# Kernel tuning notes

Measured on AMD Instinct MI355X. Metric: run time of the kernel, lower is better.

Reference implementation:

```python
import jax, jax.numpy as jnp
import numpy as np

CONV_DIMS = (-3, -2)   # spatial dims (channel-last layout)
RADIUS = (3, 3)        # window = 1 + 2*r = 7 per dim -> 49 cells
STEP = (1, 1)


def _unfold(x, dim, window, step):
    """torch.Tensor.unfold: dim -> out_len, window appended as last axis."""
    dim = dim % x.ndim
    n = x.shape[dim]
    starts = jnp.arange((n - window) // step + 1) * step          # [L]
    idx = starts[:, None] + jnp.arange(window)[None, :]           # [L, w]
    y = jnp.take(x, idx, axis=dim)                                # dim -> [L, w]
    return jnp.moveaxis(y, dim + 1, -1)                           # window axis to last


def _local_attention(x):
    # Unfold each conv dim; move its window axis to the front (as in the torch code).
    for i, r, s in zip(CONV_DIMS, RADIUS, STEP):
        x = _unfold(x, i, 1 + 2 * r, s)
        x = jnp.moveaxis(x, -1, 0)
    n_win = len(CONV_DIMS)
    cells = int(np.prod(x.shape[:n_win]))
    x = x.reshape((cells,) + x.shape[n_win:])      # [cells, B, H', W', C]
    center = cells // 2                            # spatial center of the window
    q = jnp.moveaxis(x[center:center + 1], 0, -2)  # [B, H', W', 1, C]
    k = jnp.moveaxis(jnp.concatenate([x[:center], x[center + 1:]], axis=0), 0, -2)  # [B,H',W',cells-1,C]
    d = q.shape[-1]
    scores = jnp.einsum('...qc,...kc->...qk', q, k) / jnp.sqrt(jnp.asarray(d, q.dtype))
    w = jax.nn.softmax(scores, axis=-1)
    out = jnp.einsum('...qk,...kc->...qc', w, k)   # keys double as values
    return out.squeeze(-2)                          # [B, H', W', C]


def setup_inputs() -> dict:
    key = jax.random.key(0)
    X = jax.random.normal(key, (4, 64, 64, 256), dtype=jnp.float32)
    return {"X": X}


def reference(X):
    return _local_attention(X)
```

## Files before the change

### kernel.cpp

```cpp
#include <hip/hip_runtime.h>

#define B_   4
#define H_   64
#define W_   64
#define C_   256
#define HO_  58
#define WO_  58
#define TI_  29
#define TJ_  29
#define GRID (B_ * TI_ * TJ_)

template <int CTRL>
__device__ __forceinline__ float dpp_add(float p) {
    int t = __builtin_amdgcn_update_dpp(0, __builtin_bit_cast(int, p),
                                        CTRL, 0xF, 0xF, true);
    return p + __builtin_bit_cast(float, t);
}
__device__ __forceinline__ float reduce32_dpp(float p) {
    p = dpp_add<0x111>(p);
    p = dpp_add<0x112>(p);
    p = dpp_add<0x114>(p);
    p = dpp_add<0x118>(p);
    p = dpp_add<0x142>(p);
    return p;
}

__device__ __forceinline__ float dot8(const float4& k0, const float4& k1,
                                      const float4& q0, const float4& q1) {
    float s = k0.x * q0.x;
    s = fmaf(k0.y, q0.y, s); s = fmaf(k0.z, q0.z, s); s = fmaf(k0.w, q0.w, s);
    s = fmaf(k1.x, q1.x, s); s = fmaf(k1.y, q1.y, s); s = fmaf(k1.z, q1.z, s);
    s = fmaf(k1.w, q1.w, s);
    return s;
}

__global__ __launch_bounds__(256, 4) void convnd_attn_kernel(const float* __restrict__ X,
                                                             float* __restrict__ out) {
    __shared__ float sS[4][64];
    __shared__ float sW[4][64];
    __shared__ __align__(16) float pacc[4][8][C_];

    const int xcd = blockIdx.x & 7;
    const int bt  = blockIdx.x >> 3;
    const int sp  = (xcd < 4) ? (xcd * 421 + bt) : (4 * 421 + (xcd - 4) * 420 + bt);
    const int tj  = sp % TJ_;
    const int tmp = sp / TJ_;
    const int ti  = tmp % TI_;
    const int b   = tmp / TI_;
    const int i0  = 2 * ti;
    const int j0  = 2 * tj;

    const int tid  = threadIdx.x;
    const int wave = tid >> 6;
    const int lane = tid & 63;
    const int g    = lane >> 5;
    const int sub  = lane & 31;
    const int slot = wave * 2 + g;
    const int co   = 8 * sub;

    const float* base = X + (size_t)b * (H_ * W_ * C_);

    float4 kv[8][2];
    #pragma unroll
    for (int r = 0; r < 8; ++r) {
        const float* kp = base + ((i0 + r) * W_ + (j0 + slot)) * C_ + co;
        kv[r][0] = *(const float4*)(kp);
        kv[r][1] = *(const float4*)(kp + 4);
    }

    float4 q[4][2];
    #pragma unroll
    for (int p = 0; p < 4; ++p) {
        const int a = p >> 1, c = p & 1;
        const float* qp = base + ((i0 + a + 3) * W_ + (j0 + c + 3)) * C_ + co;
        float4 q0 = *(const float4*)(qp);
        float4 q1 = *(const float4*)(qp + 4);
        q0.x *= 0.0625f; q0.y *= 0.0625f; q0.z *= 0.0625f; q0.w *= 0.0625f;
        q1.x *= 0.0625f; q1.y *= 0.0625f; q1.z *= 0.0625f; q1.w *= 0.0625f;
        q[p][0] = q0; q[p][1] = q1;
    }

    #pragma unroll
    for (int r = 0; r < 8; ++r) {
        #pragma unroll
        for (int p = 0; p < 4; ++p) {
            float s = dot8(kv[r][0], kv[r][1], q[p][0], q[p][1]);
            s = reduce32_dpp(s);
            if (sub == 31) sS[p][r * 8 + slot] = s;
        }
    }
    __syncthreads();

    {
        const int p  = wave;
        const int a  = p >> 1, c = p & 1;
        const int di = lane >> 3, dj = lane & 7;
        const bool valid = (di >= a) & (di <= a + 6) & (dj >= c) & (dj <= c + 6)
                           & !((di == a + 3) & (dj == c + 3));
        const float e = valid ? __expf(sS[p][lane]) : 0.f;
        float ts = e;
        #pragma unroll
        for (int m = 32; m; m >>= 1) ts += __shfl_xor(ts, m, 64);
        sW[p][lane] = e / ts;
    }
    __syncthreads();

    float4 acc[4][2];
    #pragma unroll
    for (int p = 0; p < 4; ++p) {
        acc[p][0] = make_float4(0.f, 0.f, 0.f, 0.f);
        acc[p][1] = make_float4(0.f, 0.f, 0.f, 0.f);
    }
    #pragma unroll
    for (int r = 0; r < 8; ++r) {
        #pragma unroll
        for (int p = 0; p < 4; ++p) {
            const float w = sW[p][r * 8 + slot];
            acc[p][0].x = fmaf(w, kv[r][0].x, acc[p][0].x);
            acc[p][0].y = fmaf(w, kv[r][0].y, acc[p][0].y);
            acc[p][0].z = fmaf(w, kv[r][0].z, acc[p][0].z);
            acc[p][0].w = fmaf(w, kv[r][0].w, acc[p][0].w);
            acc[p][1].x = fmaf(w, kv[r][1].x, acc[p][1].x);
            acc[p][1].y = fmaf(w, kv[r][1].y, acc[p][1].y);
            acc[p][1].z = fmaf(w, kv[r][1].z, acc[p][1].z);
            acc[p][1].w = fmaf(w, kv[r][1].w, acc[p][1].w);
        }
    }
    #pragma unroll
    for (int p = 0; p < 4; ++p) {
        *(float4*)&pacc[p][slot][co]     = acc[p][0];
        *(float4*)&pacc[p][slot][co + 4] = acc[p][1];
    }
    __syncthreads();

    #pragma unroll
    for (int p = 0; p < 4; ++p) {
        float s = 0.f;
        #pragma unroll
        for (int sl = 0; sl < 8; ++sl) s += pacc[p][sl][tid];
        const int a = p >> 1, c = p & 1;
        out[(((size_t)b * HO_ + (i0 + a)) * WO_ + (j0 + c)) * C_ + tid] = s;
    }
}

extern "C" void kernel_launch(void* const* d_in, const int* in_sizes, int n_in,
                              void* d_out, int out_size, void* d_ws, size_t ws_size,
                              hipStream_t stream) {
    const float* X = (const float*)d_in[0];
    float* outp    = (float*)d_out;
    hipLaunchKernelGGL(convnd_attn_kernel,
                       dim3(GRID), dim3(256), 0, stream, X, outp);
}
```

Before: 88.70 us.

## Split key rows across two wave halves with 512-thread blocks

Doubles the block to 512 threads so each half of the waves handles four of the eight key rows. This halves the per-thread key registers and FMA work. Partial accumulators from the two halves are merged in shared memory, which adds a barrier and an LDS read-modify-write pass. The final reduction and store are spread over all 512 threads. The aim is more latency hiding and lower register pressure, at the cost of extra synchronization and some idle waves during the softmax step.

Result: no change. 89.66 us (+1.1%).

```diff
diff --git a/kernel.cpp b/kernel.cpp
--- a/kernel.cpp
+++ b/kernel.cpp
@@ -34,7 +34,7 @@
     return s;
 }
 
-__global__ __launch_bounds__(256, 4) void convnd_attn_kernel(const float* __restrict__ X,
+__global__ __launch_bounds__(512, 4) void convnd_attn_kernel(const float* __restrict__ X,
                                                              float* __restrict__ out) {
     __shared__ float sS[4][64];
     __shared__ float sW[4][64];
@@ -55,15 +55,17 @@
     const int lane = tid & 63;
     const int g    = lane >> 5;
     const int sub  = lane & 31;
-    const int slot = wave * 2 + g;
+    const int rh   = wave >> 2;
+    const int col  = 2 * (wave & 3) + g;
     const int co   = 8 * sub;
 
     const float* base = X + (size_t)b * (H_ * W_ * C_);
 
-    float4 kv[8][2];
+    float4 kv[4][2];
     #pragma unroll
-    for (int r = 0; r < 8; ++r) {
-        const float* kp = base + ((i0 + r) * W_ + (j0 + slot)) * C_ + co;
+    for (int r = 0; r < 4; ++r) {
+        const int row = rh * 4 + r;
+        const float* kp = base + ((i0 + row) * W_ + (j0 + col)) * C_ + co;
         kv[r][0] = *(const float4*)(kp);
         kv[r][1] = *(const float4*)(kp + 4);
     }
@@ -81,17 +83,17 @@
     }
 
     #pragma unroll
-    for (int r = 0; r < 8; ++r) {
+    for (int r = 0; r < 4; ++r) {
         #pragma unroll
         for (int p = 0; p < 4; ++p) {
             float s = dot8(kv[r][0], kv[r][1], q[p][0], q[p][1]);
             s = reduce32_dpp(s);
-            if (sub == 31) sS[p][r * 8 + slot] = s;
+            if (sub == 31) sS[p][(rh * 4 + r) * 8 + col] = s;
         }
     }
     __syncthreads();
 
-    {
+    if (wave < 4) {
         const int p  = wave;
         const int a  = p >> 1, c = p & 1;
         const int di = lane >> 3, dj = lane & 7;
@@ -112,10 +114,10 @@
         acc[p][1] = make_float4(0.f, 0.f, 0.f, 0.f);
     }
     #pragma unroll
-    for (int r = 0; r < 8; ++r) {
+    for (int r = 0; r < 4; ++r) {
         #pragma unroll
         for (int p = 0; p < 4; ++p) {
-            const float w = sW[p][r * 8 + slot];
+            const float w = sW[p][(rh * 4 + r) * 8 + col];
             acc[p][0].x = fmaf(w, kv[r][0].x, acc[p][0].x);
             acc[p][0].y = fmaf(w, kv[r][0].y, acc[p][0].y);
             acc[p][0].z = fmaf(w, kv[r][0].z, acc[p][0].z);
@@ -126,20 +128,38 @@
             acc[p][1].w = fmaf(w, kv[r][1].w, acc[p][1].w);
         }
     }
-    #pragma unroll
-    for (int p = 0; p < 4; ++p) {
-        *(float4*)&pacc[p][slot][co]     = acc[p][0];
-        *(float4*)&pacc[p][slot][co + 4] = acc[p][1];
+
+    if (rh == 1) {
+        #pragma unroll
+        for (int p = 0; p < 4; ++p) {
+            *(float4*)&pacc[p][col][co]     = acc[p][0];
+            *(float4*)&pacc[p][col][co + 4] = acc[p][1];
+        }
+    }
+    __syncthreads();
+    if (rh == 0) {
+        #pragma unroll
+        for (int p = 0; p < 4; ++p) {
+            float4 t0 = *(const float4*)&pacc[p][col][co];
+            float4 t1 = *(const float4*)&pacc[p][col][co + 4];
+            t0.x += acc[p][0].x; t0.y += acc[p][0].y; t0.z += acc[p][0].z; t0.w += acc[p][0].w;
+            t1.x += acc[p][1].x; t1.y += acc[p][1].y; t1.z += acc[p][1].z; t1.w += acc[p][1].w;
+            *(float4*)&pacc[p][col][co]     = t0;
+            *(float4*)&pacc[p][col][co + 4] = t1;
+        }
     }
     __syncthreads();
 
+    const int ch = tid & 255;
+    const int ph = tid >> 8;
     #pragma unroll
-    for (int p = 0; p < 4; ++p) {
+    for (int pp = 0; pp < 2; ++pp) {
+        const int p = pp * 2 + ph;
         float s = 0.f;
         #pragma unroll
-        for (int sl = 0; sl < 8; ++sl) s += pacc[p][sl][tid];
+        for (int sl = 0; sl < 8; ++sl) s += pacc[p][sl][ch];
         const int a = p >> 1, c = p & 1;
-        out[(((size_t)b * HO_ + (i0 + a)) * WO_ + (j0 + c)) * C_ + tid] = s;
+        out[(((size_t)b * HO_ + (i0 + a)) * WO_ + (j0 + c)) * C_ + ch] = s;
     }
 }
 
@@ -149,5 +169,5 @@
     const float* X = (const float*)d_in[0];
     float* outp    = (float*)d_out;
     hipLaunchKernelGGL(convnd_attn_kernel,
-                       dim3(GRID), dim3(256), 0, stream, X, outp);
+                       dim3(GRID), dim3(512), 0, stream, X, outp);
 }
```

## Compute local attention with split-bf16 MFMA over 2x8 output tiles

Applied to the files above, without the earlier changes.

Each block now handles a 2x8 tile of output pixels instead of 2x2. It loads the shared 8x16 key/value patch into LDS as hi/lo bf16 pairs and computes both the scores and the weighted sum with 16x16x32 bf16 MFMA, using three products per step to emulate fp32 precision. The larger tile reuses each loaded key row across more queries and moves the dot products onto matrix cores. In exchange it adds split and convert work, swizzled LDS traffic, more barriers and lower occupancy, and the dropped lo*lo term slightly reduces precision. The last column tile overlaps the previous one (j0=50) and recomputes a few pixels.

Result: slower. 102.5 us (+15.5%).

```diff
diff --git a/kernel.cpp b/kernel.cpp
--- a/kernel.cpp
+++ b/kernel.cpp
@@ -7,139 +7,233 @@
 #define HO_  58
 #define WO_  58
 #define TI_  29
-#define TJ_  29
+#define TJ_  8
 #define GRID (B_ * TI_ * TJ_)
 
-template <int CTRL>
-__device__ __forceinline__ float dpp_add(float p) {
-    int t = __builtin_amdgcn_update_dpp(0, __builtin_bit_cast(int, p),
-                                        CTRL, 0xF, 0xF, true);
-    return p + __builtin_bit_cast(float, t);
-}
-__device__ __forceinline__ float reduce32_dpp(float p) {
-    p = dpp_add<0x111>(p);
-    p = dpp_add<0x112>(p);
-    p = dpp_add<0x114>(p);
-    p = dpp_add<0x118>(p);
-    p = dpp_add<0x142>(p);
-    return p;
-}
-
-__device__ __forceinline__ float dot8(const float4& k0, const float4& k1,
-                                      const float4& q0, const float4& q1) {
-    float s = k0.x * q0.x;
-    s = fmaf(k0.y, q0.y, s); s = fmaf(k0.z, q0.z, s); s = fmaf(k0.w, q0.w, s);
-    s = fmaf(k1.x, q1.x, s); s = fmaf(k1.y, q1.y, s); s = fmaf(k1.z, q1.z, s);
-    s = fmaf(k1.w, q1.w, s);
-    return s;
-}
-
-__global__ __launch_bounds__(256, 4) void convnd_attn_kernel(const float* __restrict__ X,
+typedef __attribute__((ext_vector_type(8))) short bf16x8;
+typedef __attribute__((ext_vector_type(4))) float f32x4;
+
+__device__ __forceinline__ void split2(float a, float b, unsigned& hi, unsigned& lo) {
+    unsigned ua = __builtin_bit_cast(unsigned, a);
+    unsigned ub = __builtin_bit_cast(unsigned, b);
+    hi = (ua >> 16) | (ub & 0xFFFF0000u);
+    float ra = a - __builtin_bit_cast(float, ua & 0xFFFF0000u);
+    float rb = b - __builtin_bit_cast(float, ub & 0xFFFF0000u);
+    lo = (__builtin_bit_cast(unsigned, ra) >> 16) |
+         (__builtin_bit_cast(unsigned, rb) & 0xFFFF0000u);
+}
+
+__device__ __forceinline__ bf16x8 ldfrag(const short* arr, int row, int col, int rowBytes) {
+    int byte = (row * rowBytes + col * 2) ^ ((row & 7) << 4);
+    return *(const bf16x8*)((const char*)arr + byte);
+}
+
+__global__ __launch_bounds__(256, 3) void convnd_attn_kernel(const float* __restrict__ X,
                                                              float* __restrict__ out) {
-    __shared__ float sS[4][64];
-    __shared__ float sW[4][64];
-    __shared__ __align__(16) float pacc[4][8][C_];
-
-    const int xcd = blockIdx.x & 7;
-    const int bt  = blockIdx.x >> 3;
-    const int sp  = (xcd < 4) ? (xcd * 421 + bt) : (4 * 421 + (xcd - 4) * 420 + bt);
-    const int tj  = sp % TJ_;
-    const int tmp = sp / TJ_;
-    const int ti  = tmp % TI_;
-    const int b   = tmp / TI_;
-    const int i0  = 2 * ti;
-    const int j0  = 2 * tj;
+    __shared__ __align__(16) short UVh[128 * 64];
+    __shared__ __align__(16) short UVl[128 * 64];
+    __shared__ __align__(16) short Wh[16 * 128];
+    __shared__ __align__(16) short Wl[16 * 128];
+    __shared__ __align__(16) float SQ[128 * 16];
+    __shared__ float psum[256];
+    __shared__ float rtot[16];
+    short* Qhi = (short*)SQ;
+    short* Qlo = Qhi + 16 * 64;
+    float* S   = SQ;
+
+    const int sp  = (blockIdx.x & 7) * 116 + (blockIdx.x >> 3);
+    const int tj  = sp & 7;
+    const int rst = sp >> 3;
+    const int ti  = rst % TI_;
+    const int b   = rst / TI_;
+    const int i0  = ti * 2;
+    const int j0  = (tj < 7) ? tj * 8 : 50;
 
     const int tid  = threadIdx.x;
     const int wave = tid >> 6;
     const int lane = tid & 63;
-    const int g    = lane >> 5;
-    const int sub  = lane & 31;
-    const int slot = wave * 2 + g;
-    const int co   = 8 * sub;
+    const int lr   = lane & 15;
+    const int kb8  = (lane >> 4) << 3;
 
     const float* base = X + (size_t)b * (H_ * W_ * C_);
 
-    float4 kv[8][2];
+    f32x4 accS0 = {0.f, 0.f, 0.f, 0.f};
+    f32x4 accS1 = {0.f, 0.f, 0.f, 0.f};
+
+    const int ucell = tid >> 1;
+    const int uhalf = (tid & 1) << 5;
+    const int ur = ucell >> 4, uc = ucell & 15;
+    const int ucol = min(j0 + uc, 63);
+    const float* usrc0 = base + (((i0 + ur) * W_) + ucol) * C_ + uhalf;
+    const int urb = ucell * 128 + uhalf * 2;
+    const int usw = (ucell & 7) << 4;
+
+    const int qpx = tid >> 4;
+    const int qc4 = (tid & 15) << 2;
+    const int qa = qpx >> 3, qb = qpx & 7;
+    const float* qsrc0 = base + (((i0 + qa + 3) * W_) + (j0 + qb + 3)) * C_ + qc4;
+    const int qrb = qpx * 128 + qc4 * 2;
+    const int qsw = (qpx & 7) << 4;
+
     #pragma unroll
-    for (int r = 0; r < 8; ++r) {
-        const float* kp = base + ((i0 + r) * W_ + (j0 + slot)) * C_ + co;
-        kv[r][0] = *(const float4*)(kp);
-        kv[r][1] = *(const float4*)(kp + 4);
-    }
-
-    float4 q[4][2];
+    for (int kc = 0; kc < 4; ++kc) {
+        {
+            const float* src = usrc0 + kc * 64;
+            float4 xx[8];
+            #pragma unroll
+            for (int e = 0; e < 8; ++e) xx[e] = *(const float4*)(src + e * 4);
+            #pragma unroll
+            for (int g = 0; g < 4; ++g) {
+                uint4 hi, lo;
+                split2(xx[g*2].x,   xx[g*2].y,   hi.x, lo.x);
+                split2(xx[g*2].z,   xx[g*2].w,   hi.y, lo.y);
+                split2(xx[g*2+1].x, xx[g*2+1].y, hi.z, lo.z);
+                split2(xx[g*2+1].z, xx[g*2+1].w, hi.w, lo.w);
+                *(uint4*)((char*)UVh + ((urb + g * 16) ^ usw)) = hi;
+                *(uint4*)((char*)UVl + ((urb + g * 16) ^ usw)) = lo;
+            }
+        }
+        {
+            float4 qx = *(const float4*)(qsrc0 + kc * 64);
+            qx.x *= 0.0625f; qx.y *= 0.0625f; qx.z *= 0.0625f; qx.w *= 0.0625f;
+            unsigned h0, l0, h1, l1;
+            split2(qx.x, qx.y, h0, l0);
+            split2(qx.z, qx.w, h1, l1);
+            *(uint2*)((char*)Qhi + (qrb ^ qsw)) = make_uint2(h0, h1);
+            *(uint2*)((char*)Qlo + (qrb ^ qsw)) = make_uint2(l0, l1);
+        }
+        __syncthreads();
+
+        #pragma unroll
+        for (int ks = 0; ks < 2; ++ks) {
+            const int kcol = ks * 32 + kb8;
+            bf16x8 qh = ldfrag(Qhi, lr, kcol, 128);
+            bf16x8 ql = ldfrag(Qlo, lr, kcol, 128);
+            {
+                const int crow = (wave * 2 + 0) * 16 + lr;
+                bf16x8 uh = ldfrag(UVh, crow, kcol, 128);
+                bf16x8 ul = ldfrag(UVl, crow, kcol, 128);
+                accS0 = __builtin_amdgcn_mfma_f32_16x16x32_bf16(uh, qh, accS0, 0, 0, 0);
+                accS0 = __builtin_amdgcn_mfma_f32_16x16x32_bf16(uh, ql, accS0, 0, 0, 0);
+                accS0 = __builtin_amdgcn_mfma_f32_16x16x32_bf16(ul, qh, accS0, 0, 0, 0);
+            }
+            {
+                const int crow = (wave * 2 + 1) * 16 + lr;
+                bf16x8 uh = ldfrag(UVh, crow, kcol, 128);
+                bf16x8 ul = ldfrag(UVl, crow, kcol, 128);
+                accS1 = __builtin_amdgcn_mfma_f32_16x16x32_bf16(uh, qh, accS1, 0, 0, 0);
+                accS1 = __builtin_amdgcn_mfma_f32_16x16x32_bf16(uh, ql, accS1, 0, 0, 0);
+                accS1 = __builtin_amdgcn_mfma_f32_16x16x32_bf16(ul, qh, accS1, 0, 0, 0);
+            }
+        }
+        __syncthreads();
+    }
+
+    {
+        const int mrow = (lane >> 4) << 2;
+        #pragma unroll
+        for (int rr = 0; rr < 4; ++rr) {
+            S[((wave * 2 + 0) * 16 + mrow + rr) * 16 + lr] = accS0[rr];
+            S[((wave * 2 + 1) * 16 + mrow + rr) * 16 + lr] = accS1[rr];
+        }
+    }
+    __syncthreads();
+
+    const int spx = tid & 15, seg = tid >> 4;
+    {
+        const int sa = spx >> 3, sb = spx & 7;
+        float e[8]; float ps = 0.f;
+        #pragma unroll
+        for (int k = 0; k < 8; ++k) {
+            const int cell = seg * 8 + k;
+            const int cr = cell >> 4, cc = cell & 15;
+            const int di = cr - sa, dj = cc - sb;
+            const bool valid = (di >= 0) & (di <= 6) & (dj >= 0) & (dj <= 6)
+                               & !((di == 3) & (dj == 3));
+            e[k] = valid ? __expf(S[cell * 16 + spx]) : 0.f;
+            ps += e[k];
+        }
+        psum[seg * 16 + spx] = ps;
+        __syncthreads();
+        if (tid < 16) {
+            float t = 0.f;
+            #pragma unroll
+            for (int s2 = 0; s2 < 16; ++s2) t += psum[s2 * 16 + tid];
+            rtot[tid] = 1.0f / t;
+        }
+        __syncthreads();
+        const float rt = rtot[spx];
+        unsigned h0,h1,h2,h3, l0,l1,l2,l3;
+        split2(e[0]*rt, e[1]*rt, h0, l0);
+        split2(e[2]*rt, e[3]*rt, h1, l1);
+        split2(e[4]*rt, e[5]*rt, h2, l2);
+        split2(e[6]*rt, e[7]*rt, h3, l3);
+        const int wb = (spx * 256 + seg * 16) ^ ((spx & 7) << 4);
+        *(uint4*)((char*)Wh + wb) = make_uint4(h0, h1, h2, h3);
+        *(uint4*)((char*)Wl + wb) = make_uint4(l0, l1, l2, l3);
+    }
+    __syncthreads();
+
+    const int cp  = tid & 63;
+    const int chg = (tid >> 6) << 4;
+    const int vr = (cp * 2) >> 4, vc = (cp * 2) & 15;
+    const int vcol0 = min(j0 + vc, 63);
+    const int vcol1 = min(j0 + vc + 1, 63);
+    const float* vsrc0 = base + (((i0 + vr) * W_) + vcol0) * C_ + chg;
+    const float* vsrc1 = base + (((i0 + vr) * W_) + vcol1) * C_ + chg;
+
     #pragma unroll
-    for (int p = 0; p < 4; ++p) {
-        const int a = p >> 1, c = p & 1;
-        const float* qp = base + ((i0 + a + 3) * W_ + (j0 + c + 3)) * C_ + co;
-        float4 q0 = *(const float4*)(qp);
-        float4 q1 = *(const float4*)(qp + 4);
-        q0.x *= 0.0625f; q0.y *= 0.0625f; q0.z *= 0.0625f; q0.w *= 0.0625f;
-        q1.x *= 0.0625f; q1.y *= 0.0625f; q1.z *= 0.0625f; q1.w *= 0.0625f;
-        q[p][0] = q0; q[p][1] = q1;
-    }
-
-    #pragma unroll
-    for (int r = 0; r < 8; ++r) {
-        #pragma unroll
-        for (int p = 0; p < 4; ++p) {
-            float s = dot8(kv[r][0], kv[r][1], q[p][0], q[p][1]);
-            s = reduce32_dpp(s);
-            if (sub == 31) sS[p][r * 8 + slot] = s;
-        }
-    }
-    __syncthreads();
-
-    {
-        const int p  = wave;
-        const int a  = p >> 1, c = p & 1;
-        const int di = lane >> 3, dj = lane & 7;
-        const bool valid = (di >= a) & (di <= a + 6) & (dj >= c) & (dj <= c + 6)
-                           & !((di == a + 3) & (dj == c + 3));
-        const float e = valid ? __expf(sS[p][lane]) : 0.f;
-        float ts = e;
-        #pragma unroll
-        for (int m = 32; m; m >>= 1) ts += __shfl_xor(ts, m, 64);
-        sW[p][lane] = e / ts;
-    }
-    __syncthreads();
-
-    float4 acc[4][2];
-    #pragma unroll
-    for (int p = 0; p < 4; ++p) {
-        acc[p][0] = make_float4(0.f, 0.f, 0.f, 0.f);
-        acc[p][1] = make_float4(0.f, 0.f, 0.f, 0.f);
-    }
-    #pragma unroll
-    for (int r = 0; r < 8; ++r) {
-        #pragma unroll
-        for (int p = 0; p < 4; ++p) {
-            const float w = sW[p][r * 8 + slot];
-            acc[p][0].x = fmaf(w, kv[r][0].x, acc[p][0].x);
-            acc[p][0].y = fmaf(w, kv[r][0].y, acc[p][0].y);
-            acc[p][0].z = fmaf(w, kv[r][0].z, acc[p][0].z);
-            acc[p][0].w = fmaf(w, kv[r][0].w, acc[p][0].w);
-            acc[p][1].x = fmaf(w, kv[r][1].x, acc[p][1].x);
-            acc[p][1].y = fmaf(w, kv[r][1].y, acc[p][1].y);
-            acc[p][1].z = fmaf(w, kv[r][1].z, acc[p][1].z);
-            acc[p][1].w = fmaf(w, kv[r][1].w, acc[p][1].w);
-        }
-    }
-    #pragma unroll
-    for (int p = 0; p < 4; ++p) {
-        *(float4*)&pacc[p][slot][co]     = acc[p][0];
-        *(float4*)&pacc[p][slot][co + 4] = acc[p][1];
-    }
-    __syncthreads();
-
-    #pragma unroll
-    for (int p = 0; p < 4; ++p) {
-        float s = 0.f;
-        #pragma unroll
-        for (int sl = 0; sl < 8; ++sl) s += pacc[p][sl][tid];
-        const int a = p >> 1, c = p & 1;
-        out[(((size_t)b * HO_ + (i0 + a)) * WO_ + (j0 + c)) * C_ + tid] = s;
+    for (int nc = 0; nc < 4; ++nc) {
+        {
+            float4 y0[4], y1[4];
+            #pragma unroll
+            for (int e = 0; e < 4; ++e) {
+                y0[e] = *(const float4*)(vsrc0 + nc * 64 + e * 4);
+                y1[e] = *(const float4*)(vsrc1 + nc * 64 + e * 4);
+            }
+            #pragma unroll
+            for (int jj = 0; jj < 4; ++jj) {
+                const int chb = chg + jj * 4;
+                unsigned h, l;
+                split2(y0[jj].x, y1[jj].x, h, l);
+                { int by = ((chb+0) * 256 + cp * 4) ^ (((chb+0) & 7) << 4);
+                  *(unsigned*)((char*)UVh + by) = h; *(unsigned*)((char*)UVl + by) = l; }
+                split2(y0[jj].y, y1[jj].y, h, l);
+                { int by = ((chb+1) * 256 + cp * 4) ^ (((chb+1) & 7) << 4);
+                  *(unsigned*)((char*)UVh + by) = h; *(unsigned*)((char*)UVl + by) = l; }
+                split2(y0[jj].z, y1[jj].z, h, l);
+                { int by = ((chb+2) * 256 + cp * 4) ^ (((chb+2) & 7) << 4);
+                  *(unsigned*)((char*)UVh + by) = h; *(unsigned*)((char*)UVl + by) = l; }
+                split2(y0[jj].w, y1[jj].w, h, l);
+                { int by = ((chb+3) * 256 + cp * 4) ^ (((chb+3) & 7) << 4);
+                  *(unsigned*)((char*)UVh + by) = h; *(unsigned*)((char*)UVl + by) = l; }
+            }
+        }
+        __syncthreads();
+
+        f32x4 accO = {0.f, 0.f, 0.f, 0.f};
+        #pragma unroll
+        for (int ks = 0; ks < 4; ++ks) {
+            const int kcol = ks * 32 + kb8;
+            bf16x8 wh = ldfrag(Wh, lr, kcol, 256);
+            bf16x8 wl = ldfrag(Wl, lr, kcol, 256);
+            bf16x8 vh = ldfrag(UVh, wave * 16 + lr, kcol, 256);
+            bf16x8 vl = ldfrag(UVl, wave * 16 + lr, kcol, 256);
+            accO = __builtin_amdgcn_mfma_f32_16x16x32_bf16(wh, vh, accO, 0, 0, 0);
+            accO = __builtin_amdgcn_mfma_f32_16x16x32_bf16(wh, vl, accO, 0, 0, 0);
+            accO = __builtin_amdgcn_mfma_f32_16x16x32_bf16(wl, vh, accO, 0, 0, 0);
+        }
+        {
+            const int ch = nc * 64 + wave * 16 + lr;
+            const int mrow = (lane >> 4) << 2;
+            #pragma unroll
+            for (int rr = 0; rr < 4; ++rr) {
+                const int px = mrow + rr;
+                const int a = px >> 3, bb = px & 7;
+                out[(((size_t)b * HO_ + (i0 + a)) * WO_ + (j0 + bb)) * C_ + ch] = accO[rr];
+            }
+        }
+        __syncthreads();
     }
 }
 
```
